# Kernel tuning notes

Measured on AMD Instinct MI355X. Metric: run time of the kernel, lower is better.

Reference implementation:

```python
import jax, jax.numpy as jnp
import numpy as np

TAU = 2.0
VTH = 1.0
EPS = 1e-5
T_STEPS = 64

@jax.custom_vjp
def spike_atan(x):
    # Heaviside spike with ATan surrogate gradient (spikingjelly surrogate.ATan, alpha=2.0)
    return (x >= 0.0).astype(x.dtype)

def _spike_fwd(x):
    return spike_atan(x), x

def _spike_bwd(x, g):
    # d/dx [1/pi * atan(pi/2 * alpha * x) + 1/2] with alpha=2 -> 1 / (1 + (pi*x)^2)
    return (g / (1.0 + (jnp.pi * x) ** 2),)

spike_atan.defvjp(_spike_fwd, _spike_bwd)

def bn_eval(x, g, b, m, v):
    return (x - m) * (g / jnp.sqrt(v + EPS)) + b

def setup_inputs() -> dict:
    key = jax.random.key(0)
    ks = jax.random.split(key, 16)
    N, C, L, H, NC = 16384, 22, 63, 64, 4
    D = C * L
    s1 = 1.0 / np.sqrt(D)
    s2 = 1.0 / np.sqrt(H)
    return {
        'x': jax.random.normal(ks[0], (N, C, L), jnp.float32),
        'fc1_w': jax.random.normal(ks[1], (H, D), jnp.float32) * s1,
        'fc1_b': jax.random.normal(ks[2], (H,), jnp.float32) * s1,
        'bn1_g': jax.random.uniform(ks[3], (H,), jnp.float32, 0.5, 1.5),
        'bn1_b': jax.random.normal(ks[4], (H,), jnp.float32) * 0.1,
        'bn1_m': jax.random.normal(ks[5], (H,), jnp.float32) * 0.1,
        'bn1_v': jax.random.uniform(ks[6], (H,), jnp.float32, 0.5, 1.5),
        'fc2_w': jax.random.normal(ks[7], (H, H), jnp.float32) * s2,
        'fc2_b': jax.random.normal(ks[8], (H,), jnp.float32) * s2,
        'bn2_g': jax.random.uniform(ks[9], (H,), jnp.float32, 0.5, 1.5),
        'bn2_b': jax.random.normal(ks[10], (H,), jnp.float32) * 0.1,
        'bn2_m': jax.random.normal(ks[11], (H,), jnp.float32) * 0.1,
        'bn2_v': jax.random.uniform(ks[12], (H,), jnp.float32, 0.5, 1.5),
        'cls_w': jax.random.normal(ks[13], (NC, H), jnp.float32) * s2,
        'cls_b': jax.random.normal(ks[14], (NC,), jnp.float32) * s2,
    }

def reference(x, fc1_w, fc1_b, bn1_g, bn1_b, bn1_m, bn1_v,
              fc2_w, fc2_b, bn2_g, bn2_b, bn2_m, bn2_v, cls_w, cls_b):
    N = x.shape[0]
    x_flat = x.reshape(N, -1)                       # [N, 1386]
    # fc1+bn1 input is identical every timestep -> compute once
    a1 = bn_eval(x_flat @ fc1_w.T + fc1_b, bn1_g, bn1_b, bn1_m, bn1_v)  # [N, 64]

    def step(carry, _):
        v1, v2 = carry
        # LIF 1 (decay_input=True, hard reset to 0)
        h1 = v1 + (a1 - v1) / TAU
        s1 = spike_atan(h1 - VTH)
        v1n = h1 * (1.0 - s1)
        # fc2 + bn2 (eval mode; dropout inactive in inference)
        z = bn_eval(s1 @ fc2_w.T + fc2_b, bn2_g, bn2_b, bn2_m, bn2_v)
        # LIF 2
        h2 = v2 + (z - v2) / TAU
        s2 = spike_atan(h2 - VTH)
        v2n = h2 * (1.0 - s2)
        return (v1n, v2n), s2

    v0 = jnp.zeros_like(a1)
    _, out_seq = jax.lax.scan(step, (v0, v0), None, length=T_STEPS)  # [T, N, 64]
    logits = jnp.einsum('tnh,ch->tnc', out_seq, cls_w) + cls_b        # [T, N, 4]
    return logits.mean(axis=0)                                        # [N, 4]
```

## Files before the change

kernel.cpp:

```cpp
#include <hip/hip_runtime.h>
#include <hip/hip_bf16.h>

#define D_IN 1386
#define EPS 1e-5f
#define CHUNKS 44

typedef __attribute__((ext_vector_type(8))) short short8v;
typedef __attribute__((ext_vector_type(4))) float f32x4;
typedef unsigned short ushortt;

__device__ inline unsigned short bf16rne(float f) {
    unsigned int u = __float_as_uint(f);
    u += 0x7FFFu + ((u >> 16) & 1u);
    return (unsigned short)(u >> 16);
}
__device__ inline float bfbits_to_f(unsigned short b) {
    return __uint_as_float(((unsigned int)b) << 16);
}

union S8U { short8v s; unsigned int u[4]; };

__device__ inline unsigned int cvt2(float v0, float v1, float& r0, float& r1) {
    union { __hip_bfloat162 b2; unsigned int u; } cv;
    cv.b2 = __float22bfloat162_rn(make_float2(v0, v1));
    r0 = v0 - __uint_as_float((cv.u & 0xFFFFu) << 16);
    r1 = v1 - __uint_as_float(cv.u & 0xFFFF0000u);
    return cv.u;
}
__device__ inline unsigned int cvt2n(float v0, float v1) {
    union { __hip_bfloat162 b2; unsigned int u; } cv;
    cv.b2 = __float22bfloat162_rn(make_float2(v0, v1));
    return cv.u;
}

__global__ __launch_bounds__(256) void prep_w3(const float* __restrict__ w,
                                               ushortt* __restrict__ w3) {
    int idx = blockIdx.x * 256 + threadIdx.x;
    if (idx >= CHUNKS * 6144) return;
    int c   = idx / 6144;
    int rem = idx - c * 6144;
    int g   = rem >> 9;
    int l   = (rem >> 3) & 63;
    int j   = rem & 7;
    int T   = g / 3, s = g - 3 * T;
    int h   = 16 * T + (l & 15);
    int k   = 32 * c + 8 * (l >> 4) + j;
    float v = (k < D_IN) ? w[h * D_IN + k] : 0.f;
    unsigned short hh = bf16rne(v);
    float r1 = v - bfbits_to_f(hh);
    unsigned short mm = bf16rne(r1);
    float r2 = r1 - bfbits_to_f(mm);
    unsigned short ll = bf16rne(r2);
    w3[idx] = (s == 0) ? hh : (s == 1) ? mm : ll;
}

__global__ __launch_bounds__(512, 4) void fc1_mfma(const float* __restrict__ x,
                                                   const ushortt* __restrict__ w3,
                                                   float* __restrict__ y) {
    const int lane = threadIdx.x & 63;
    const int wid  = threadIdx.x >> 6;
    const int T    = wid & 3;
    const int mt   = wid >> 2;
    const int n0   = blockIdx.x * 32 + mt * 16;
    const int r    = lane & 15;
    const int g4   = lane >> 4;
    const float* xrow = x + (size_t)(n0 + r) * D_IN + 8 * g4;
    const ushortt* wT = w3 + 3 * T * 512;

    f32x4 acc = (f32x4){0.f, 0.f, 0.f, 0.f};

    float aE[8], aO[8];
    short8v BE[3], BO[3];

    auto loadAx = [&](int c, float (&a)[8]) {
        if (c < CHUNKS - 1) {
            const float2* p = (const float2*)(xrow + 32 * c);
#pragma unroll
            for (int i = 0; i < 4; ++i) {
                float2 v = p[i]; a[2 * i] = v.x; a[2 * i + 1] = v.y;
            }
        } else {
#pragma unroll
            for (int j = 0; j < 8; ++j) {
                int kk = 8 * g4 + j;
                a[j] = (kk < D_IN - 32 * (CHUNKS - 1)) ? xrow[32 * (CHUNKS - 1) + j] : 0.f;
            }
        }
    };
    auto loadBx = [&](int c, short8v (&B)[3]) {
        const short8v* bp = (const short8v*)(wT + (size_t)c * 6144) + lane;
#pragma unroll
        for (int s = 0; s < 3; ++s) B[s] = bp[s * 64];
    };
    auto body = [&](float (&a)[8], short8v (&B)[3]) {
        S8U Ah, Am, Al;
#pragma unroll
        for (int d = 0; d < 4; ++d) {
            float m0, m1, l0, l1;
            Ah.u[d] = cvt2(a[2 * d], a[2 * d + 1], m0, m1);
            Am.u[d] = cvt2(m0, m1, l0, l1);
            Al.u[d] = cvt2n(l0, l1);
        }
        const short8v XH = Ah.s, XM = Am.s, XL = Al.s;
        const short8v Bh = B[0], Bm = B[1], Bl = B[2];
        acc = __builtin_amdgcn_mfma_f32_16x16x32_bf16(XL, Bh, acc, 0, 0, 0);
        acc = __builtin_amdgcn_mfma_f32_16x16x32_bf16(XM, Bm, acc, 0, 0, 0);
        acc = __builtin_amdgcn_mfma_f32_16x16x32_bf16(XH, Bl, acc, 0, 0, 0);
        acc = __builtin_amdgcn_mfma_f32_16x16x32_bf16(XM, Bh, acc, 0, 0, 0);
        acc = __builtin_amdgcn_mfma_f32_16x16x32_bf16(XH, Bm, acc, 0, 0, 0);
        acc = __builtin_amdgcn_mfma_f32_16x16x32_bf16(XH, Bh, acc, 0, 0, 0);
    };

    loadAx(0, aE); loadBx(0, BE);
    loadAx(1, aO); loadBx(1, BO);

    for (int j = 0; j < CHUNKS / 2; ++j) {
        body(aE, BE);
        if (2 * j + 2 < CHUNKS) { loadAx(2 * j + 2, aE); loadBx(2 * j + 2, BE); }
        body(aO, BO);
        if (2 * j + 3 < CHUNKS) { loadAx(2 * j + 3, aO); loadBx(2 * j + 3, BO); }
    }

#pragma unroll
    for (int q = 0; q < 4; ++q)
        y[(size_t)(n0 + 4 * g4 + q) * 64 + 16 * T + r] = acc[q];
}

__global__ __launch_bounds__(256, 4) void snn_kernel(
    const float* __restrict__ y,
    const float* __restrict__ fc1_b,
    const float* __restrict__ bn1_g, const float* __restrict__ bn1_b,
    const float* __restrict__ bn1_m, const float* __restrict__ bn1_v,
    const float* __restrict__ fc2_w, const float* __restrict__ fc2_b,
    const float* __restrict__ bn2_g, const float* __restrict__ bn2_b,
    const float* __restrict__ bn2_m, const float* __restrict__ bn2_v,
    const float* __restrict__ cls_w, const float* __restrict__ cls_b,
    float* __restrict__ out)
{
    __shared__ unsigned int spk[2][16][36];
    __shared__ float redc[4][16][4];
    const int lane = threadIdx.x & 63;
    const int T    = threadIdx.x >> 6;
    const int n0   = blockIdx.x * 16;
    const int r    = lane & 15;
    const int grp  = lane >> 4;

    short8v Whi[2], Wlo[2];
    {
        const int hp = 16 * T + r;
        const float scale = bn2_g[hp] / sqrtf(bn2_v[hp] + EPS);
#pragma unroll
        for (int Hh = 0; Hh < 2; ++Hh) {
            S8U hi, lo;
#pragma unroll
            for (int d = 0; d < 4; ++d) {
                const int kk = 32 * Hh + 8 * grp + 2 * d;
                float w0 = fc2_w[hp * 64 + kk]     * scale;
                float w1 = fc2_w[hp * 64 + kk + 1] * scale;
                unsigned short h0 = bf16rne(w0), h1 = bf16rne(w1);
                unsigned short l0 = bf16rne(w0 - bfbits_to_f(h0));
                unsigned short l1 = bf16rne(w1 - bfbits_to_f(h1));
                hi.u[d] = (unsigned int)h0 | ((unsigned int)h1 << 16);
                lo.u[d] = (unsigned int)l0 | ((unsigned int)l1 << 16);
            }
            Whi[Hh] = hi.s;
            Wlo[Hh] = lo.s;
        }
    }

    const int h0 = 16 * T + 4 * grp;
    float a1[4], biasD[4];
    {
        float4 yv = *(const float4*)&y[(size_t)(n0 + r) * 64 + h0];
#pragma unroll
        for (int q = 0; q < 4; ++q) {
            const int h = h0 + q;
            float s1v = bn1_g[h] / sqrtf(bn1_v[h] + EPS);
            float yq  = (q == 0) ? yv.x : (q == 1) ? yv.y : (q == 2) ? yv.z : yv.w;
            a1[q] = (yq + fc1_b[h] - bn1_m[h]) * s1v + bn1_b[h];
            const float s2v = bn2_g[h] / sqrtf(bn2_v[h] + EPS);
            biasD[q] = (fc2_b[h] - bn2_m[h]) * s2v + bn2_b[h];
        }
    }

    float v1[4], v2[4], cnt[4];
#pragma unroll
    for (int q = 0; q < 4; ++q) { v1[q] = 0.f; v2[q] = 0.f; cnt[q] = 0.f; }

    for (int t = 0; t < 64; ++t) {
        const int b = t & 1;
        unsigned int dw0, dw1;
        {
            float h1a = v1[0] + (a1[0] - v1[0]) * 0.5f;
            float h1b = v1[1] + (a1[1] - v1[1]) * 0.5f;
            float h1c = v1[2] + (a1[2] - v1[2]) * 0.5f;
            float h1d = v1[3] + (a1[3] - v1[3]) * 0.5f;
            bool sa = h1a >= 1.f, sb = h1b >= 1.f, sc = h1c >= 1.f, sd = h1d >= 1.f;
            v1[0] = sa ? 0.f : h1a; v1[1] = sb ? 0.f : h1b;
            v1[2] = sc ? 0.f : h1c; v1[3] = sd ? 0.f : h1d;
            dw0 = (sa ? 0x3F80u : 0u) | (sb ? 0x3F800000u : 0u);
            dw1 = (sc ? 0x3F80u : 0u) | (sd ? 0x3F800000u : 0u);
        }
        *(uint2*)&spk[b][r][8 * T + 2 * grp] = make_uint2(dw0, dw1);
        __syncthreads();
        uint4 wv0 = *(const uint4*)&spk[b][r][4 * grp];
        uint4 wv1 = *(const uint4*)&spk[b][r][16 + 4 * grp];
        S8U s0u, s1u;
        s0u.u[0] = wv0.x; s0u.u[1] = wv0.y; s0u.u[2] = wv0.z; s0u.u[3] = wv0.w;
        s1u.u[0] = wv1.x; s1u.u[1] = wv1.y; s1u.u[2] = wv1.z; s1u.u[3] = wv1.w;
        const short8v S0 = s0u.s, S1 = s1u.s;

        f32x4 c1;
        c1[0] = biasD[0]; c1[1] = biasD[1]; c1[2] = biasD[2]; c1[3] = biasD[3];
        f32x4 c2 = (f32x4){0.f, 0.f, 0.f, 0.f};
        c1 = __builtin_amdgcn_mfma_f32_16x16x32_bf16(Whi[0], S0, c1, 0, 0, 0);
        c2 = __builtin_amdgcn_mfma_f32_16x16x32_bf16(Wlo[0], S0, c2, 0, 0, 0);
        c1 = __builtin_amdgcn_mfma_f32_16x16x32_bf16(Whi[1], S1, c1, 0, 0, 0);
        c2 = __builtin_amdgcn_mfma_f32_16x16x32_bf16(Wlo[1], S1, c2, 0, 0, 0);

#pragma unroll
        for (int q = 0; q < 4; ++q) {
            float z  = c1[q] + c2[q];
            float h2 = v2[q] + (z - v2[q]) * 0.5f;
            bool s = h2 >= 1.f;
            v2[q] = s ? 0.f : h2;
            cnt[q] += s ? 1.f : 0.f;
        }
    }

    float p[4];
#pragma unroll
    for (int c = 0; c < 4; ++c) {
        p[c] = cnt[0] * cls_w[c * 64 + h0]     + cnt[1] * cls_w[c * 64 + h0 + 1]
             + cnt[2] * cls_w[c * 64 + h0 + 2] + cnt[3] * cls_w[c * 64 + h0 + 3];
        p[c] += __shfl_xor(p[c], 16);
        p[c] += __shfl_xor(p[c], 32);
    }
    if (lane < 16) {
        float4 v; v.x = p[0]; v.y = p[1]; v.z = p[2]; v.w = p[3];
        *(float4*)&redc[T][lane][0] = v;
    }
    __syncthreads();
    if (threadIdx.x < 16) {
        const int s = threadIdx.x;
        float4 o;
        o.x = (redc[0][s][0] + redc[1][s][0] + redc[2][s][0] + redc[3][s][0]) * (1.f / 64.f) + cls_b[0];
        o.y = (redc[0][s][1] + redc[1][s][1] + redc[2][s][1] + redc[3][s][1]) * (1.f / 64.f) + cls_b[1];
        o.z = (redc[0][s][2] + redc[1][s][2] + redc[2][s][2] + redc[3][s][2]) * (1.f / 64.f) + cls_b[2];
        o.w = (redc[0][s][3] + redc[1][s][3] + redc[2][s][3] + redc[3][s][3]) * (1.f / 64.f) + cls_b[3];
        *(float4*)&out[(size_t)(n0 + s) * 4] = o;
    }
}

extern "C" void kernel_launch(void* const* d_in, const int* in_sizes, int n_in,
                              void* d_out, int out_size, void* d_ws, size_t ws_size,
                              hipStream_t stream) {
    const float* x     = (const float*)d_in[0];
    const float* fc1_w = (const float*)d_in[1];
    const float* fc1_b = (const float*)d_in[2];
    const float* bn1_g = (const float*)d_in[3];
    const float* bn1_b = (const float*)d_in[4];
    const float* bn1_m = (const float*)d_in[5];
    const float* bn1_v = (const float*)d_in[6];
    const float* fc2_w = (const float*)d_in[7];
    const float* fc2_b = (const float*)d_in[8];
    const float* bn2_g = (const float*)d_in[9];
    const float* bn2_b = (const float*)d_in[10];
    const float* bn2_m = (const float*)d_in[11];
    const float* bn2_v = (const float*)d_in[12];
    const float* cls_w = (const float*)d_in[13];
    const float* cls_b = (const float*)d_in[14];

    float*   y  = (float*)d_ws;
    ushortt* w3 = (ushortt*)((char*)d_ws + (4 << 20));

    prep_w3 <<<1056, 256, 0, stream>>>(fc1_w, w3);
    fc1_mfma<<<512,  512, 0, stream>>>(x, w3, y);
    snn_kernel<<<1024, 256, 0, stream>>>(y, fc1_b, bn1_g, bn1_b, bn1_m, bn1_v,
                                         fc2_w, fc2_b, bn2_g, bn2_b, bn2_m, bn2_v,
                                         cls_w, cls_b, (float*)d_out);
}
```

Before: 90.30 us.

## Stage fc1 operands through double-buffered LDS and split K across two blocks

The fc1 MFMA kernel now stages each K chunk of the pre-split bf16 weights and the x tile through a double-buffered shared-memory buffer. All four waves reuse the same x bf16 hi/mid/lo split instead of each wave converting it separately. The K dimension is split in half across paired blocks, which write partial sums to two workspace slabs that the SNN kernel adds together, doubling the grid. In exchange the kernel adds block-level barriers every chunk, LDS traffic and a second partial-y buffer that has to be read.

```diff
diff --git a/kernel.cpp b/kernel.cpp
--- a/kernel.cpp
+++ b/kernel.cpp
@@ -4,6 +4,7 @@
 #define D_IN 1386
 #define EPS 1e-5f
 #define CHUNKS 44
+#define KHALF 22
 
 typedef __attribute__((ext_vector_type(8))) short short8v;
 typedef __attribute__((ext_vector_type(4))) float f32x4;
@@ -54,76 +55,106 @@
     w3[idx] = (s == 0) ? hh : (s == 1) ? mm : ll;
 }
 
-__global__ __launch_bounds__(512, 4) void fc1_mfma(const float* __restrict__ x,
+__global__ __launch_bounds__(256, 4) void fc1_mfma(const float* __restrict__ x,
                                                    const ushortt* __restrict__ w3,
-                                                   float* __restrict__ y) {
-    const int lane = threadIdx.x & 63;
-    const int wid  = threadIdx.x >> 6;
-    const int T    = wid & 3;
-    const int mt   = wid >> 2;
-    const int n0   = blockIdx.x * 32 + mt * 16;
+                                                   float* __restrict__ ypart) {
+    __shared__ ushortt lds[2][9216];
+    const int t    = threadIdx.x;
+    const int lane = t & 63;
+    const int T    = t >> 6;
+    const int kh   = blockIdx.x & 1;
+    const int sb   = blockIdx.x >> 1;
+    const int n0   = sb * 32;
+    const int c0   = kh * KHALF;
     const int r    = lane & 15;
     const int g4   = lane >> 4;
-    const float* xrow = x + (size_t)(n0 + r) * D_IN + 8 * g4;
-    const ushortt* wT = w3 + 3 * T * 512;
-
-    f32x4 acc = (f32x4){0.f, 0.f, 0.f, 0.f};
-
-    float aE[8], aO[8];
-    short8v BE[3], BO[3];
-
-    auto loadAx = [&](int c, float (&a)[8]) {
+    const int row  = t >> 3;
+    const int u    = t & 7;
+    const int sgw  = row >> 4;
+    const int lanew = (row & 15) + 16 * (u >> 1);
+    const int half = u & 1;
+    const float* xp0 = x + (size_t)(n0 + row) * D_IN + 4 * u;
+
+    f32x4 acc[2];
+    acc[0] = (f32x4){0.f, 0.f, 0.f, 0.f};
+    acc[1] = (f32x4){0.f, 0.f, 0.f, 0.f};
+
+    uint4 bB[3];
+    float xf[4];
+
+    auto stage_load = [&](int c) {
+        const ushortt* wp = w3 + (size_t)c * 6144 + t * 8;
+        bB[0] = *(const uint4*)(wp);
+        bB[1] = *(const uint4*)(wp + 2048);
+        bB[2] = *(const uint4*)(wp + 4096);
+        const float* xp = xp0 + 32 * c;
         if (c < CHUNKS - 1) {
-            const float2* p = (const float2*)(xrow + 32 * c);
-#pragma unroll
-            for (int i = 0; i < 4; ++i) {
-                float2 v = p[i]; a[2 * i] = v.x; a[2 * i + 1] = v.y;
-            }
+            float2 v0 = *(const float2*)xp;
+            float2 v1 = *(const float2*)(xp + 2);
+            xf[0] = v0.x; xf[1] = v0.y; xf[2] = v1.x; xf[3] = v1.y;
         } else {
-#pragma unroll
-            for (int j = 0; j < 8; ++j) {
-                int kk = 8 * g4 + j;
-                a[j] = (kk < D_IN - 32 * (CHUNKS - 1)) ? xrow[32 * (CHUNKS - 1) + j] : 0.f;
-            }
+            const int k0 = 32 * c + 4 * u;
+#pragma unroll
+            for (int e = 0; e < 4; ++e)
+                xf[e] = (k0 + e < D_IN) ? xp[e] : 0.f;
         }
     };
-    auto loadBx = [&](int c, short8v (&B)[3]) {
-        const short8v* bp = (const short8v*)(wT + (size_t)c * 6144) + lane;
-#pragma unroll
-        for (int s = 0; s < 3; ++s) B[s] = bp[s * 64];
+    auto stage_write = [&](int nb) {
+#pragma unroll
+        for (int i = 0; i < 3; ++i)
+            *(uint4*)&lds[nb][i * 2048 + t * 8] = bB[i];
+        float m0, m1, m2, m3, l0, l1, l2, l3;
+        unsigned int h01 = cvt2(xf[0], xf[1], m0, m1);
+        unsigned int h23 = cvt2(xf[2], xf[3], m2, m3);
+        unsigned int q01 = cvt2(m0, m1, l0, l1);
+        unsigned int q23 = cvt2(m2, m3, l2, l3);
+        unsigned int w01 = cvt2n(l0, l1);
+        unsigned int w23 = cvt2n(l2, l3);
+        ushortt* ab = &lds[nb][6144 + sgw * 1536 + lanew * 8 + half * 4];
+        *(uint2*)(ab)         = make_uint2(h01, h23);
+        *(uint2*)(ab + 512)   = make_uint2(q01, q23);
+        *(uint2*)(ab + 1024)  = make_uint2(w01, w23);
     };
-    auto body = [&](float (&a)[8], short8v (&B)[3]) {
-        S8U Ah, Am, Al;
-#pragma unroll
-        for (int d = 0; d < 4; ++d) {
-            float m0, m1, l0, l1;
-            Ah.u[d] = cvt2(a[2 * d], a[2 * d + 1], m0, m1);
-            Am.u[d] = cvt2(m0, m1, l0, l1);
-            Al.u[d] = cvt2n(l0, l1);
-        }
-        const short8v XH = Ah.s, XM = Am.s, XL = Al.s;
-        const short8v Bh = B[0], Bm = B[1], Bl = B[2];
-        acc = __builtin_amdgcn_mfma_f32_16x16x32_bf16(XL, Bh, acc, 0, 0, 0);
-        acc = __builtin_amdgcn_mfma_f32_16x16x32_bf16(XM, Bm, acc, 0, 0, 0);
-        acc = __builtin_amdgcn_mfma_f32_16x16x32_bf16(XH, Bl, acc, 0, 0, 0);
-        acc = __builtin_amdgcn_mfma_f32_16x16x32_bf16(XM, Bh, acc, 0, 0, 0);
-        acc = __builtin_amdgcn_mfma_f32_16x16x32_bf16(XH, Bm, acc, 0, 0, 0);
-        acc = __builtin_amdgcn_mfma_f32_16x16x32_bf16(XH, Bh, acc, 0, 0, 0);
+    auto compute = [&](int cb) {
+        const ushortt* base = &lds[cb][0];
+        const short8v Bh = *(const short8v*)(base + (3 * T + 0) * 512 + lane * 8);
+        const short8v Bm = *(const short8v*)(base + (3 * T + 1) * 512 + lane * 8);
+        const short8v Bl = *(const short8v*)(base + (3 * T + 2) * 512 + lane * 8);
+#pragma unroll
+        for (int sg = 0; sg < 2; ++sg) {
+            const ushortt* ab = base + 6144 + sg * 1536 + lane * 8;
+            const short8v XH = *(const short8v*)(ab);
+            const short8v XM = *(const short8v*)(ab + 512);
+            const short8v XL = *(const short8v*)(ab + 1024);
+            f32x4 c = acc[sg];
+            c = __builtin_amdgcn_mfma_f32_16x16x32_bf16(XL, Bh, c, 0, 0, 0);
+            c = __builtin_amdgcn_mfma_f32_16x16x32_bf16(XM, Bm, c, 0, 0, 0);
+            c = __builtin_amdgcn_mfma_f32_16x16x32_bf16(XH, Bl, c, 0, 0, 0);
+            c = __builtin_amdgcn_mfma_f32_16x16x32_bf16(XM, Bh, c, 0, 0, 0);
+            c = __builtin_amdgcn_mfma_f32_16x16x32_bf16(XH, Bm, c, 0, 0, 0);
+            c = __builtin_amdgcn_mfma_f32_16x16x32_bf16(XH, Bh, c, 0, 0, 0);
+            acc[sg] = c;
+        }
     };
 
-    loadAx(0, aE); loadBx(0, BE);
-    loadAx(1, aO); loadBx(1, BO);
-
-    for (int j = 0; j < CHUNKS / 2; ++j) {
-        body(aE, BE);
-        if (2 * j + 2 < CHUNKS) { loadAx(2 * j + 2, aE); loadBx(2 * j + 2, BE); }
-        body(aO, BO);
-        if (2 * j + 3 < CHUNKS) { loadAx(2 * j + 3, aO); loadBx(2 * j + 3, BO); }
-    }
-
-#pragma unroll
-    for (int q = 0; q < 4; ++q)
-        y[(size_t)(n0 + 4 * g4 + q) * 64 + 16 * T + r] = acc[q];
+    stage_load(c0);
+    stage_write(0);
+    __syncthreads();
+
+    for (int i = 0; i < KHALF; ++i) {
+        const int cb = i & 1;
+        if (i + 1 < KHALF) stage_load(c0 + i + 1);
+        compute(cb);
+        if (i + 1 < KHALF) stage_write(cb ^ 1);
+        __syncthreads();
+    }
+
+    float* yp = ypart + (size_t)kh * (16384 * 64);
+#pragma unroll
+    for (int sg = 0; sg < 2; ++sg)
+#pragma unroll
+        for (int q = 0; q < 4; ++q)
+            yp[(size_t)(n0 + sg * 16 + 4 * g4 + q) * 64 + 16 * T + r] = acc[sg][q];
 }
 
 __global__ __launch_bounds__(256, 4) void snn_kernel(
@@ -171,12 +202,14 @@
     const int h0 = 16 * T + 4 * grp;
     float a1[4], biasD[4];
     {
-        float4 yv = *(const float4*)&y[(size_t)(n0 + r) * 64 + h0];
+        float4 ya = *(const float4*)&y[(size_t)(n0 + r) * 64 + h0];
+        float4 yb = *(const float4*)&y[(size_t)16384 * 64 + (size_t)(n0 + r) * 64 + h0];
 #pragma unroll
         for (int q = 0; q < 4; ++q) {
             const int h = h0 + q;
             float s1v = bn1_g[h] / sqrtf(bn1_v[h] + EPS);
-            float yq  = (q == 0) ? yv.x : (q == 1) ? yv.y : (q == 2) ? yv.z : yv.w;
+            float yq  = (q == 0) ? ya.x + yb.x : (q == 1) ? ya.y + yb.y
+                      : (q == 2) ? ya.z + yb.z : ya.w + yb.w;
             a1[q] = (yq + fc1_b[h] - bn1_m[h]) * s1v + bn1_b[h];
             const float s2v = bn2_g[h] / sqrtf(bn2_v[h] + EPS);
             biasD[q] = (fc2_b[h] - bn2_m[h]) * s2v + bn2_b[h];
@@ -271,12 +304,12 @@
     const float* cls_w = (const float*)d_in[13];
     const float* cls_b = (const float*)d_in[14];
 
-    float*   y  = (float*)d_ws;
-    ushortt* w3 = (ushortt*)((char*)d_ws + (4 << 20));
+    float*   ypart = (float*)d_ws;
+    ushortt* w3    = (ushortt*)((char*)d_ws + (8 << 20));
 
     prep_w3 <<<1056, 256, 0, stream>>>(fc1_w, w3);
-    fc1_mfma<<<512,  512, 0, stream>>>(x, w3, y);
-    snn_kernel<<<1024, 256, 0, stream>>>(y, fc1_b, bn1_g, bn1_b, bn1_m, bn1_v,
+    fc1_mfma<<<1024, 256, 0, stream>>>(x, w3, ypart);
+    snn_kernel<<<1024, 256, 0, stream>>>(ypart, fc1_b, bn1_g, bn1_b, bn1_m, bn1_v,
                                          fc2_w, fc2_b, bn2_g, bn2_b, bn2_m, bn2_v,
                                          cls_w, cls_b, (float*)d_out);
 }
```

New measurement: 125.0 us. 38.4% more time.
